# Kernel tuning notes

Measured on AMD Instinct MI355X. Metric: run time of the kernel, lower is better.

Reference implementation:

```python
import jax, jax.numpy as jnp
import numpy as np

B, N, C = 4, 2048, 768
H = 12
D = C // H  # head_dim = 64
SCALE = D ** -0.5


def setup_inputs() -> dict:
    key = jax.random.key(0)
    ks = jax.random.split(key, 9)
    x_q = jax.random.normal(ks[0], (B, N, C), dtype=jnp.float32)
    x_k = jax.random.normal(ks[1], (B, N, C), dtype=jnp.float32)
    x_v = jax.random.normal(ks[2], (B, N, C), dtype=jnp.float32)
    x_u = jax.random.uniform(ks[3], (B, N, C), dtype=jnp.float32)
    s = C ** -0.5
    Wq = jax.random.normal(ks[4], (C, C), dtype=jnp.float32) * s
    Wk = jax.random.normal(ks[5], (C, C), dtype=jnp.float32) * s
    Wv = jax.random.normal(ks[6], (C, C), dtype=jnp.float32) * s
    Wp = jax.random.normal(ks[7], (C, C), dtype=jnp.float32) * s
    bp = jax.random.normal(ks[8], (C,), dtype=jnp.float32) * 0.01
    return {"x_q": x_q, "x_k": x_k, "x_v": x_v, "x_u": x_u,
            "Wq": Wq, "Wk": Wk, "Wv": Wv, "Wp": Wp, "bp": bp}


def reference(x_q, x_k, x_v, x_u, Wq, Wk, Wv, Wp, bp):
    # Linear projections (torch Linear: y = x @ W.T), split into heads [B,H,N,D]
    def to_heads(x, W):
        y = jnp.einsum('bnc,oc->bno', x, W)
        return y.reshape(B, N, H, D).transpose(0, 2, 1, 3)
    q = to_heads(x_q, Wq) * SCALE
    k = to_heads(x_k, Wk)
    v = to_heads(x_v, Wv)
    # Scores [B,H,N,N]
    attn = jnp.einsum('bhqd,bhkd->bhqk', q, k)
    # Uncertainty map: per-query scalar (mean over channels), broadcast over keys & heads
    uc = jnp.mean(x_u, axis=-1)  # [B,N]
    attn = attn * uc[:, None, :, None]
    attn = jax.nn.softmax(attn, axis=-1)
    out = jnp.einsum('bhqk,bhkd->bhqd', attn, v)
    out = out.transpose(0, 2, 1, 3).reshape(B, N, C)
    return jnp.einsum('bnc,oc->bno', out, Wp) + bp
```

## Files before the change

### kernel.cpp

```cpp
#include <hip/hip_runtime.h>
#include <hip/hip_bf16.h>
#include <cstdint>

#define B_ 4
#define N_ 2048
#define C_ 768
#define H_ 12
#define D_ 64
#define QSCALE 0.18033688011112042f

typedef __bf16 bf16x8 __attribute__((ext_vector_type(8)));
typedef float f32x4 __attribute__((ext_vector_type(4)));

__device__ __forceinline__ unsigned f2bs(float x) {
  unsigned u = __builtin_bit_cast(unsigned, x);
  unsigned r = (u + 0x7fffu + ((u >> 16) & 1u)) >> 16;
  return r;
}

__device__ __forceinline__ bf16x8 ldb8(const unsigned short* p) {
  return __builtin_bit_cast(bf16x8, *(const uint4*)p);
}

__device__ __forceinline__ f32x4 mfma16(bf16x8 a, bf16x8 b, f32x4 c) {
  return __builtin_amdgcn_mfma_f32_16x16x32_bf16(a, b, c, 0, 0, 0);
}

__device__ __forceinline__ void async16(const unsigned short* g, unsigned short* l) {
  __builtin_amdgcn_global_load_lds(
      (const __attribute__((address_space(1))) unsigned int*)g,
      (__attribute__((address_space(3))) unsigned int*)l, 16, 0, 0);
}

__global__ void convx_kernel(const float* __restrict__ s0, const float* __restrict__ s1,
                             const float* __restrict__ s2,
                             unsigned short* __restrict__ d0, unsigned short* __restrict__ d1,
                             unsigned short* __restrict__ d2) {
  const float* s; unsigned short* d;
  switch (blockIdx.y) {
    case 0: s = s0; d = d0; break;
    case 1: s = s1; d = d1; break;
    default: s = s2; d = d2; break;
  }
  int i = (blockIdx.x * 256 + threadIdx.x) * 4;
  float4 v = *(const float4*)(s + i);
  ushort4 h;
  h.x = (unsigned short)f2bs(v.x); h.y = (unsigned short)f2bs(v.y);
  h.z = (unsigned short)f2bs(v.z); h.w = (unsigned short)f2bs(v.w);
  *(ushort4*)(d + i) = h;
}

__global__ void convw_kernel(const float* __restrict__ s0, const float* __restrict__ s1,
                             const float* __restrict__ s2, const float* __restrict__ s3,
                             unsigned short* __restrict__ d0, unsigned short* __restrict__ d1,
                             unsigned short* __restrict__ d2, unsigned short* __restrict__ d3) {
  const float* s; unsigned short* d;
  switch (blockIdx.y) {
    case 0: s = s0; d = d0; break;
    case 1: s = s1; d = d1; break;
    case 2: s = s2; d = d2; break;
    default: s = s3; d = d3; break;
  }
  int i = (blockIdx.x * 256 + threadIdx.x) * 4;
  float4 v = *(const float4*)(s + i);
  ushort4 h;
  h.x = (unsigned short)f2bs(v.x); h.y = (unsigned short)f2bs(v.y);
  h.z = (unsigned short)f2bs(v.z); h.w = (unsigned short)f2bs(v.w);
  *(ushort4*)(d + i) = h;
}

__global__ void uc_kernel(const float* __restrict__ xu, float* __restrict__ uc) {
  int w = threadIdx.x >> 6, lane = threadIdx.x & 63;
  int row = blockIdx.x * 4 + w;
  const float* p = xu + (size_t)row * C_;
  float s = 0.f;
#pragma unroll
  for (int i = 0; i < 3; ++i) {
    float4 v = *(const float4*)(p + (i * 64 + lane) * 4);
    s += v.x + v.y + v.z + v.w;
  }
#pragma unroll
  for (int off = 1; off < 64; off <<= 1) s += __shfl_xor(s, off);
  if (lane == 0) uc[row] = s * (1.f / 768.f);
}

__device__ __forceinline__ void gemm_mainloop(
    const unsigned short* __restrict__ A, const unsigned short* __restrict__ W,
    int m0, int n0, unsigned short* Al, unsigned short* Bl,
    int tid, int wm, int wn, int quad, int id15, f32x4 (*acc)[4]) {
  const int wb = tid & 192;
  int rows[4], cols[4];
#pragma unroll
  for (int s = 0; s < 4; ++s) {
    int g = s * 256 + tid;
    rows[s] = (g >> 2) & 127;
    cols[s] = ((g >> 9) << 5) | ((g & 3) << 3);
  }
  const unsigned short* ap[4];
  const unsigned short* bp[4];
#pragma unroll
  for (int s = 0; s < 4; ++s) {
    ap[s] = A + (size_t)(m0 + rows[s]) * C_ + cols[s];
    bp[s] = W + (size_t)(n0 + rows[s]) * C_ + cols[s];
  }

  for (int kt = 0; kt < C_; kt += 64) {
    __syncthreads();
#pragma unroll
    for (int s = 0; s < 4; ++s) {
      async16(ap[s] + kt, Al + (s * 256 + wb) * 8);
      async16(bp[s] + kt, Bl + (s * 256 + wb) * 8);
    }
    __syncthreads();

#pragma unroll
    for (int kk = 0; kk < 2; ++kk) {
      bf16x8 af[4], bfr[4];
#pragma unroll
      for (int i = 0; i < 4; ++i)
        af[i]  = ldb8(&Al[kk * 4096 + (wm + i * 16 + id15) * 32 + quad * 8]);
#pragma unroll
      for (int j = 0; j < 4; ++j)
        bfr[j] = ldb8(&Bl[kk * 4096 + (wn + j * 16 + id15) * 32 + quad * 8]);
#pragma unroll
      for (int i = 0; i < 4; ++i)
#pragma unroll
        for (int j = 0; j < 4; ++j)
          acc[i][j] = mfma16(af[i], bfr[j], acc[i][j]);
    }
  }
}

__global__ __launch_bounds__(256, 3) void gemm_qkv(
    const unsigned short* __restrict__ xq, const unsigned short* __restrict__ xk,
    const unsigned short* __restrict__ xv,
    const unsigned short* __restrict__ wq, const unsigned short* __restrict__ wk,
    const unsigned short* __restrict__ wv,
    unsigned short* __restrict__ oq, unsigned short* __restrict__ ok,
    unsigned short* __restrict__ ov, const float* __restrict__ uc) {
  __shared__ __align__(16) unsigned short Al[128 * 64];
  __shared__ __align__(16) unsigned short Bl[128 * 64];
  const int tid = threadIdx.x;
  const int w = tid >> 6, lane = tid & 63, quad = lane >> 4, id15 = lane & 15;
  const int wm = (w >> 1) << 6, wn = (w & 1) << 6;
  const int m0 = blockIdx.y << 7, n0 = blockIdx.x << 7;
  const int z = blockIdx.z;

  const unsigned short* A = (z == 0) ? xq : (z == 1) ? xk : xv;
  const unsigned short* W = (z == 0) ? wq : (z == 1) ? wk : wv;

  f32x4 acc[4][4] = {};
  gemm_mainloop(A, W, m0, n0, Al, Bl, tid, wm, wn, quad, id15, acc);

#pragma unroll
  for (int i = 0; i < 4; ++i) {
#pragma unroll
    for (int j = 0; j < 4; ++j) {
#pragma unroll
      for (int r = 0; r < 4; ++r) {
        int gm = m0 + wm + i * 16 + quad * 4 + r;
        int gn = n0 + wn + j * 16 + id15;
        float v = acc[i][j][r];
        if (z == 0) {
          v *= QSCALE * uc[gm];
          oq[(size_t)gm * C_ + gn] = (unsigned short)f2bs(v);
        } else if (z == 1) {
          ok[(size_t)gm * C_ + gn] = (unsigned short)f2bs(v);
        } else {
          int b = gm >> 11, n = gm & (N_ - 1);
          ov[(size_t)(b * C_ + gn) * N_ + n] = (unsigned short)f2bs(v);
        }
      }
    }
  }
}

__global__ __launch_bounds__(256, 3) void gemm_out(
    const unsigned short* __restrict__ ao, const unsigned short* __restrict__ wp,
    float* __restrict__ out, const float* __restrict__ bias) {
  __shared__ __align__(16) unsigned short Al[128 * 64];
  __shared__ __align__(16) unsigned short Bl[128 * 64];
  const int tid = threadIdx.x;
  const int w = tid >> 6, lane = tid & 63, quad = lane >> 4, id15 = lane & 15;
  const int wm = (w >> 1) << 6, wn = (w & 1) << 6;
  const int m0 = blockIdx.y << 7, n0 = blockIdx.x << 7;

  f32x4 acc[4][4] = {};
  gemm_mainloop(ao, wp, m0, n0, Al, Bl, tid, wm, wn, quad, id15, acc);

#pragma unroll
  for (int i = 0; i < 4; ++i) {
#pragma unroll
    for (int j = 0; j < 4; ++j) {
#pragma unroll
      for (int r = 0; r < 4; ++r) {
        int gm = m0 + wm + i * 16 + quad * 4 + r;
        int gn = n0 + wn + j * 16 + id15;
        out[(size_t)gm * C_ + gn] = acc[i][j][r] + bias[gn];
      }
    }
  }
}

#define KSTR 72
#define PSTR 72
__global__ __launch_bounds__(256, 3) void attn_kernel(
    const unsigned short* __restrict__ Q, const unsigned short* __restrict__ Kk,
    const unsigned short* __restrict__ Vt, unsigned short* __restrict__ O) {
  __shared__ __align__(16) unsigned short Kl[64 * KSTR];
  __shared__ __align__(16) unsigned short Vl[64 * KSTR];
  __shared__ __align__(16) unsigned short Pl[8][16 * PSTR];

  const int tid = threadIdx.x;
  const int w = tid >> 6, lane = tid & 63, quad = lane >> 4, id15 = lane & 15;
  const int bh = blockIdx.y;
  const int b = bh / H_, h = bh % H_;
  const int q0 = blockIdx.x * 128 + w * 32;

  bf16x8 qf[2][2];
#pragma unroll
  for (int rg = 0; rg < 2; ++rg)
#pragma unroll
    for (int kb = 0; kb < 2; ++kb)
      qf[rg][kb] = ldb8(Q + (size_t)(b * N_ + q0 + rg * 16 + id15) * C_ + h * 64 + kb * 32 + quad * 8);

  const uint4 onesu = {0x3F803F80u, 0x3F803F80u, 0x3F803F80u, 0x3F803F80u};
  const bf16x8 onesf = __builtin_bit_cast(bf16x8, onesu);

  f32x4 oacc[2][4] = {};
  f32x4 lacc[2] = {};

  const size_t kbase = (size_t)(b * N_) * C_ + h * 64;
  const size_t vbase = (size_t)(b * C_ + h * 64) * N_;
  const int srow0 = tid >> 3, srow1 = (256 + tid) >> 3;
  const int sseg0 = (tid & 7) << 3;

  unsigned short* Plw0 = &Pl[w * 2 + 0][0];
  unsigned short* Plw1 = &Pl[w * 2 + 1][0];

  for (int kc = 0; kc < N_; kc += 64) {
    __syncthreads();
    *(uint4*)&Kl[srow0 * KSTR + sseg0] = *(const uint4*)(Kk + kbase + (size_t)(kc + srow0) * C_ + sseg0);
    *(uint4*)&Kl[srow1 * KSTR + sseg0] = *(const uint4*)(Kk + kbase + (size_t)(kc + srow1) * C_ + sseg0);
    *(uint4*)&Vl[srow0 * KSTR + sseg0] = *(const uint4*)(Vt + vbase + (size_t)srow0 * N_ + kc + sseg0);
    *(uint4*)&Vl[srow1 * KSTR + sseg0] = *(const uint4*)(Vt + vbase + (size_t)srow1 * N_ + kc + sseg0);
    __syncthreads();

    f32x4 sA[4], sB[4];
#pragma unroll
    for (int cb = 0; cb < 4; ++cb) {
      f32x4 a = {}, c = {};
#pragma unroll
      for (int kb = 0; kb < 2; ++kb) {
        bf16x8 kf = ldb8(&Kl[(cb * 16 + id15) * KSTR + kb * 32 + quad * 8]);
        a = mfma16(kf, qf[0][kb], a);
        c = mfma16(kf, qf[1][kb], c);
      }
      sA[cb] = a; sB[cb] = c;
    }

#pragma unroll
    for (int rg = 0; rg < 2; ++rg) {
      f32x4* s4 = (rg == 0) ? sA : sB;
      unsigned short* Plw = (rg == 0) ? Plw0 : Plw1;
#pragma unroll
      for (int cb = 0; cb < 4; ++cb) {
        unsigned p0 = __builtin_bit_cast(unsigned, exp2f(s4[cb][0]));
        unsigned p1 = __builtin_bit_cast(unsigned, exp2f(s4[cb][1]));
        unsigned p2 = __builtin_bit_cast(unsigned, exp2f(s4[cb][2]));
        unsigned p3 = __builtin_bit_cast(unsigned, exp2f(s4[cb][3]));
        uint2 u;
        u.x = __builtin_amdgcn_perm(p1, p0, 0x07060302u);
        u.y = __builtin_amdgcn_perm(p3, p2, 0x07060302u);
        *(uint2*)&Plw[id15 * PSTR + cb * 16 + quad * 4] = u;
      }
    }

    bf16x8 pf[2][2];
#pragma unroll
    for (int kb = 0; kb < 2; ++kb) {
      pf[0][kb] = ldb8(&Plw0[id15 * PSTR + kb * 32 + quad * 8]);
      pf[1][kb] = ldb8(&Plw1[id15 * PSTR + kb * 32 + quad * 8]);
    }

#pragma unroll
    for (int kb = 0; kb < 2; ++kb) {
      lacc[0] = mfma16(pf[0][kb], onesf, lacc[0]);
      lacc[1] = mfma16(pf[1][kb], onesf, lacc[1]);
    }
#pragma unroll
    for (int db = 0; db < 4; ++db) {
#pragma unroll
      for (int kb = 0; kb < 2; ++kb) {
        bf16x8 vf = ldb8(&Vl[(db * 16 + id15) * KSTR + kb * 32 + quad * 8]);
        oacc[0][db] = mfma16(pf[0][kb], vf, oacc[0][db]);
        oacc[1][db] = mfma16(pf[1][kb], vf, oacc[1][db]);
      }
    }
  }

#pragma unroll
  for (int rg = 0; rg < 2; ++rg) {
#pragma unroll
    for (int r = 0; r < 4; ++r) {
      float linv = 1.0f / lacc[rg][r];
      int n = q0 + rg * 16 + quad * 4 + r;
#pragma unroll
      for (int db = 0; db < 4; ++db)
        O[(size_t)(b * N_ + n) * C_ + h * 64 + db * 16 + id15] = (unsigned short)f2bs(oacc[rg][db][r] * linv);
    }
  }
}

extern "C" void kernel_launch(void* const* d_in, const int* in_sizes, int n_in,
                              void* d_out, int out_size, void* d_ws, size_t ws_size,
                              hipStream_t stream) {
  const float* x_q = (const float*)d_in[0];
  const float* x_k = (const float*)d_in[1];
  const float* x_v = (const float*)d_in[2];
  const float* x_u = (const float*)d_in[3];
  const float* Wq  = (const float*)d_in[4];
  const float* Wk  = (const float*)d_in[5];
  const float* Wv  = (const float*)d_in[6];
  const float* Wp  = (const float*)d_in[7];
  const float* bp  = (const float*)d_in[8];

  char* ws = (char*)d_ws;
  size_t off = 0;
  auto alloc = [&](size_t bytes) {
    char* p = ws + off;
    off += (bytes + 255) & ~(size_t)255;
    return p;
  };
  unsigned short* wq16 = (unsigned short*)alloc((size_t)C_ * C_ * 2);
  unsigned short* wk16 = (unsigned short*)alloc((size_t)C_ * C_ * 2);
  unsigned short* wv16 = (unsigned short*)alloc((size_t)C_ * C_ * 2);
  unsigned short* wp16 = (unsigned short*)alloc((size_t)C_ * C_ * 2);
  float*          ucp  = (float*)alloc((size_t)B_ * N_ * 4);
  unsigned short* xq16 = (unsigned short*)alloc((size_t)B_ * N_ * C_ * 2);
  unsigned short* xk16 = (unsigned short*)alloc((size_t)B_ * N_ * C_ * 2);
  unsigned short* xv16 = (unsigned short*)alloc((size_t)B_ * N_ * C_ * 2);
  unsigned short* q_s  = (unsigned short*)alloc((size_t)B_ * N_ * C_ * 2);
  unsigned short* k_s  = (unsigned short*)alloc((size_t)B_ * N_ * C_ * 2);
  unsigned short* vT   = (unsigned short*)alloc((size_t)B_ * N_ * C_ * 2);
  unsigned short* ao   = (unsigned short*)alloc((size_t)B_ * N_ * C_ * 2);

  convx_kernel<<<dim3(6144, 3), 256, 0, stream>>>(x_q, x_k, x_v, xq16, xk16, xv16);
  convw_kernel<<<dim3(576, 4), 256, 0, stream>>>(Wq, Wk, Wv, Wp, wq16, wk16, wv16, wp16);
  uc_kernel<<<dim3(2048), 256, 0, stream>>>(x_u, ucp);
  gemm_qkv<<<dim3(6, 64, 3), 256, 0, stream>>>(xq16, xk16, xv16, wq16, wk16, wv16,
                                               q_s, k_s, vT, ucp);
  attn_kernel<<<dim3(16, 48), 256, 0, stream>>>(q_s, k_s, vT, ao);
  gemm_out<<<dim3(6, 64), 256, 0, stream>>>(ao, wp16, (float*)d_out, bp);
}
```

Before: 335.8 us.

## Register-prefetch next tiles in GEMM and attention loops to overlap loads with MFMA

```diff
diff --git a/kernel.cpp b/kernel.cpp
--- a/kernel.cpp
+++ b/kernel.cpp
@@ -24,12 +24,6 @@
 
 __device__ __forceinline__ f32x4 mfma16(bf16x8 a, bf16x8 b, f32x4 c) {
   return __builtin_amdgcn_mfma_f32_16x16x32_bf16(a, b, c, 0, 0, 0);
-}
-
-__device__ __forceinline__ void async16(const unsigned short* g, unsigned short* l) {
-  __builtin_amdgcn_global_load_lds(
-      (const __attribute__((address_space(1))) unsigned int*)g,
-      (__attribute__((address_space(3))) unsigned int*)l, 16, 0, 0);
 }
 
 __global__ void convx_kernel(const float* __restrict__ s0, const float* __restrict__ s1,
@@ -88,30 +82,40 @@
     const unsigned short* __restrict__ A, const unsigned short* __restrict__ W,
     int m0, int n0, unsigned short* Al, unsigned short* Bl,
     int tid, int wm, int wn, int quad, int id15, f32x4 (*acc)[4]) {
-  const int wb = tid & 192;
-  int rows[4], cols[4];
+  const unsigned short* ap[4];
+  const unsigned short* bp[4];
 #pragma unroll
   for (int s = 0; s < 4; ++s) {
     int g = s * 256 + tid;
-    rows[s] = (g >> 2) & 127;
-    cols[s] = ((g >> 9) << 5) | ((g & 3) << 3);
-  }
-  const unsigned short* ap[4];
-  const unsigned short* bp[4];
+    int row = (g >> 2) & 127;
+    int col = ((g >> 9) << 5) | ((g & 3) << 3);
+    ap[s] = A + (size_t)(m0 + row) * C_ + col;
+    bp[s] = W + (size_t)(n0 + row) * C_ + col;
+  }
+
+  uint4 ra[4], rb[4];
 #pragma unroll
   for (int s = 0; s < 4; ++s) {
-    ap[s] = A + (size_t)(m0 + rows[s]) * C_ + cols[s];
-    bp[s] = W + (size_t)(n0 + rows[s]) * C_ + cols[s];
+    ra[s] = *(const uint4*)(ap[s]);
+    rb[s] = *(const uint4*)(bp[s]);
   }
 
   for (int kt = 0; kt < C_; kt += 64) {
     __syncthreads();
 #pragma unroll
     for (int s = 0; s < 4; ++s) {
-      async16(ap[s] + kt, Al + (s * 256 + wb) * 8);
-      async16(bp[s] + kt, Bl + (s * 256 + wb) * 8);
+      *(uint4*)&Al[(s * 256 + tid) * 8] = ra[s];
+      *(uint4*)&Bl[(s * 256 + tid) * 8] = rb[s];
     }
     __syncthreads();
+
+    if (kt + 64 < C_) {
+#pragma unroll
+      for (int s = 0; s < 4; ++s) {
+        ra[s] = *(const uint4*)(ap[s] + kt + 64);
+        rb[s] = *(const uint4*)(bp[s] + kt + 64);
+      }
+    }
 
 #pragma unroll
     for (int kk = 0; kk < 2; ++kk) {
@@ -235,16 +239,33 @@
   const int srow0 = tid >> 3, srow1 = (256 + tid) >> 3;
   const int sseg0 = (tid & 7) << 3;
 
+  const unsigned short* kp0 = Kk + kbase + (size_t)srow0 * C_ + sseg0;
+  const unsigned short* kp1 = Kk + kbase + (size_t)srow1 * C_ + sseg0;
+  const unsigned short* vp0 = Vt + vbase + (size_t)srow0 * N_ + sseg0;
+  const unsigned short* vp1 = Vt + vbase + (size_t)srow1 * N_ + sseg0;
+
   unsigned short* Plw0 = &Pl[w * 2 + 0][0];
   unsigned short* Plw1 = &Pl[w * 2 + 1][0];
 
+  uint4 rk0 = *(const uint4*)(kp0);
+  uint4 rk1 = *(const uint4*)(kp1);
+  uint4 rv0 = *(const uint4*)(vp0);
+  uint4 rv1 = *(const uint4*)(vp1);
+
   for (int kc = 0; kc < N_; kc += 64) {
     __syncthreads();
-    *(uint4*)&Kl[srow0 * KSTR + sseg0] = *(const uint4*)(Kk + kbase + (size_t)(kc + srow0) * C_ + sseg0);
-    *(uint4*)&Kl[srow1 * KSTR + sseg0] = *(const uint4*)(Kk + kbase + (size_t)(kc + srow1) * C_ + sseg0);
-    *(uint4*)&Vl[srow0 * KSTR + sseg0] = *(const uint4*)(Vt + vbase + (size_t)srow0 * N_ + kc + sseg0);
-    *(uint4*)&Vl[srow1 * KSTR + sseg0] = *(const uint4*)(Vt + vbase + (size_t)srow1 * N_ + kc + sseg0);
+    *(uint4*)&Kl[srow0 * KSTR + sseg0] = rk0;
+    *(uint4*)&Kl[srow1 * KSTR + sseg0] = rk1;
+    *(uint4*)&Vl[srow0 * KSTR + sseg0] = rv0;
+    *(uint4*)&Vl[srow1 * KSTR + sseg0] = rv1;
     __syncthreads();
+
+    if (kc + 64 < N_) {
+      rk0 = *(const uint4*)(kp0 + (size_t)(kc + 64) * C_);
+      rk1 = *(const uint4*)(kp1 + (size_t)(kc + 64) * C_);
+      rv0 = *(const uint4*)(vp0 + (kc + 64));
+      rv1 = *(const uint4*)(vp1 + (kc + 64));
+    }
 
     f32x4 sA[4], sB[4];
 #pragma unroll
```

Measured after the change: 499.1 us. 48.6% more time.
